# Performance work log

Measured on AMD Instinct MI355X. Metric: run time of the kernel, lower is better.

Reference implementation:

```python
import jax, jax.numpy as jnp
import numpy as np

N_NODES = 50000
N_EDGES = 800000
IN_DIM = 128
HID = 32
HEADS = 4
OUT_DIM = 128
NEG_SLOPE = 0.2


def setup_inputs() -> dict:
    key = jax.random.key(0)
    ks = jax.random.split(key, 10)
    s = lambda fan_in: 1.0 / np.sqrt(fan_in)
    return {
        "x": jax.random.normal(ks[0], (N_NODES, IN_DIM), dtype=jnp.float32),
        "edge_index": jax.random.randint(ks[1], (2, N_EDGES), 0, N_NODES, dtype=jnp.int64),
        # encoder GATConv: in=IN_DIM, out=HID, heads=HEADS (concat)
        "W1": jax.random.normal(ks[2], (IN_DIM, HEADS * HID), dtype=jnp.float32) * s(IN_DIM),
        "att_src1": jax.random.normal(ks[3], (HEADS, HID), dtype=jnp.float32) * s(HID),
        "att_dst1": jax.random.normal(ks[4], (HEADS, HID), dtype=jnp.float32) * s(HID),
        "b1": jnp.zeros((HEADS * HID,), dtype=jnp.float32),
        # decoder GATConv: in=HEADS*HID, out=OUT_DIM, heads=1
        "W2": jax.random.normal(ks[5], (HEADS * HID, OUT_DIM), dtype=jnp.float32) * s(HEADS * HID),
        "att_src2": jax.random.normal(ks[6], (1, OUT_DIM), dtype=jnp.float32) * s(OUT_DIM),
        "att_dst2": jax.random.normal(ks[7], (1, OUT_DIM), dtype=jnp.float32) * s(OUT_DIM),
        "b2": jnp.zeros((OUT_DIM,), dtype=jnp.float32),
    }


def _gat_conv(x, src, dst, W, att_src, att_dst, bias, heads, out_ch):
    """PyG-style GATConv (v1), eval mode (dropout off), self-loops already in src/dst."""
    n = x.shape[0]
    h = (x @ W).reshape(n, heads, out_ch)                 # [N,H,C]
    a_src = jnp.einsum("nhc,hc->nh", h, att_src)          # [N,H]
    a_dst = jnp.einsum("nhc,hc->nh", h, att_dst)          # [N,H]
    e = jax.nn.leaky_relu(a_src[src] + a_dst[dst], NEG_SLOPE)  # [E,H]
    # segment softmax over destination neighborhoods
    e_max = jax.ops.segment_max(e, dst, num_segments=n)   # [N,H]
    e_exp = jnp.exp(e - e_max[dst])
    denom = jax.ops.segment_sum(e_exp, dst, num_segments=n)
    alpha = e_exp / (denom[dst] + 1e-16)                  # [E,H]
    msg = h[src] * alpha[:, :, None]                      # [E,H,C]
    out = jax.ops.segment_sum(msg, dst, num_segments=n)   # [N,H,C]
    return out.reshape(n, heads * out_ch) + bias


def reference(x, edge_index, W1, att_src1, att_dst1, b1, W2, att_src2, att_dst2, b2):
    n = x.shape[0]
    loops = jnp.arange(n, dtype=edge_index.dtype)
    src = jnp.concatenate([edge_index[0], loops])
    dst = jnp.concatenate([edge_index[1], loops])
    z = jax.nn.relu(_gat_conv(x, src, dst, W1, att_src1, att_dst1, b1, HEADS, HID))
    x_hat = jax.nn.relu(_gat_conv(z, src, dst, W2, att_src2, att_dst2, b2, 1, OUT_DIM))
    return x_hat
```

## Files before the change

kernel.cpp:

```cpp
#include <hip/hip_runtime.h>
#include <hip/hip_bf16.h>
#include <cstddef>

#define N_NODES 50000
#define N_EDGES_RAW 800000
#define E_TOT (N_EDGES_RAW + N_NODES)
#define DIM 128
#define NEG_SLOPE 0.2f

#define NBUCK 196
#define CHUNK 4096
#define NBLK_E ((E_TOT + CHUNK - 1) / CHUNK)
#define CONV_BLKS 3125
#define GB 782

typedef __attribute__((ext_vector_type(8))) short bf16x8;
typedef __attribute__((ext_vector_type(4))) float f32x4;

__device__ __forceinline__ ushort f2bf(float f) {
  unsigned u = __float_as_uint(f);
  return (ushort)((u + 0x7FFFu + ((u >> 16) & 1u)) >> 16);
}
__device__ __forceinline__ float bf2f_lo(uint u) {
  return __uint_as_float(u << 16);
}
__device__ __forceinline__ float bf2f_hi(uint u) {
  return __uint_as_float(u & 0xFFFF0000u);
}

__device__ __forceinline__ void get_edge(const int* __restrict__ ei, int is64,
                                         int e, int& s, int& d) {
  if (e >= N_EDGES_RAW) { s = e - N_EDGES_RAW; d = s; return; }
  if (is64) {
    s = ei[2 * (size_t)e];
    d = ei[2 * ((size_t)N_EDGES_RAW + (size_t)e)];
  } else {
    s = ei[e];
    d = ei[N_EDGES_RAW + e];
  }
}

__device__ __forceinline__ int detect_inline(const int* __restrict__ ei,
                                             int* sflag) {
  const int t = threadIdx.x;
  if (t < 64) {
    int hi = ei[2 * t + 1];
    unsigned long long b = __ballot(hi != 0);
    if (t == 0) *sflag = (b == 0ULL) ? 1 : 0;
  }
  __syncthreads();
  return *sflag;
}

__device__ __forceinline__ void prep_one(const float* __restrict__ w,
                                         const float* __restrict__ atts,
                                         const float* __restrict__ attd,
                                         ushort* __restrict__ wtx,
                                         int H, int idx) {
  const int c = idx >> 7, k = idx & 127;
  const int C = 128 / H;
  float v;
  if (c < 128) {
    v = w[k * 128 + c];
  } else if (c < 128 + H) {
    const int hd = c - 128;
    float s = 0.f;
    for (int j = 0; j < C; ++j) s += w[k * 128 + hd * C + j] * atts[hd * C + j];
    v = s;
  } else if (c < 128 + 2 * H) {
    const int hd = c - 128 - H;
    float s = 0.f;
    for (int j = 0; j < C; ++j) s += w[k * 128 + hd * C + j] * attd[hd * C + j];
    v = s;
  } else {
    v = 0.f;
  }
  wtx[idx] = f2bf(v);
}

__global__ __launch_bounds__(256) void mega_setup(
    const float* __restrict__ W1, const float* __restrict__ as1,
    const float* __restrict__ ad1, ushort* __restrict__ wtx1,
    const float* __restrict__ W2, const float* __restrict__ as2,
    const float* __restrict__ ad2, ushort* __restrict__ wtx2,
    const float* __restrict__ x, ushort* __restrict__ x_bf,
    const int* __restrict__ ei, int* __restrict__ hist_mat,
    unsigned* __restrict__ pairs) {
  const int b = blockIdx.x, t = threadIdx.x;
  if (b < 72) {
    prep_one(W1, as1, ad1, wtx1, 4, b * 256 + t);
  } else if (b < 144) {
    prep_one(W2, as2, ad2, wtx2, 1, (b - 72) * 256 + t);
  } else if (b < 144 + CONV_BLKS) {
    const int base = (b - 144) * 2048 + t * 8;
    float4 v0 = *(const float4*)(x + base);
    float4 v1 = *(const float4*)(x + base + 4);
    ushort u[8];
    u[0] = f2bf(v0.x); u[1] = f2bf(v0.y); u[2] = f2bf(v0.z); u[3] = f2bf(v0.w);
    u[4] = f2bf(v1.x); u[5] = f2bf(v1.y); u[6] = f2bf(v1.z); u[7] = f2bf(v1.w);
    *(uint4*)(x_bf + base) = *(const uint4*)u;
  } else {
    __shared__ int hist[NBUCK];
    __shared__ int sflag;
    const int cb = b - 144 - CONV_BLKS;
    if (t < NBUCK) hist[t] = 0;
    const int is64 = detect_inline(ei, &sflag);
    __syncthreads();
    const int e0 = cb * CHUNK;
#pragma unroll
    for (int i = 0; i < CHUNK / 256; ++i) {
      int e = e0 + i * 256 + t;
      if (e < E_TOT) {
        int s, d;
        get_edge(ei, is64, e, s, d);
        pairs[e] = (unsigned)s | ((unsigned)d << 16);
        atomicAdd(&hist[d >> 8], 1);
      }
    }
    __syncthreads();
    if (t < NBUCK) hist_mat[cb * NBUCK + t] = hist[t];
  }
}

__global__ __launch_bounds__(256) void bucket_scatter(
    const unsigned* __restrict__ pairs, const int* __restrict__ hist_mat,
    unsigned* __restrict__ tmp, int* __restrict__ bstart_g) {
  __shared__ int wtot[4];
  __shared__ int sbase[NBUCK];
  __shared__ int shist[NBUCK];
  const int b = blockIdx.x, t = threadIdx.x, lane = t & 63, wid = t >> 6;
  int tot = 0, pre = 0;
  if (t < NBUCK) {
    for (int bb = 0; bb < NBLK_E; ++bb) {
      int v = hist_mat[bb * NBUCK + t];
      pre += (bb < b) ? v : 0;
      tot += v;
    }
    shist[t] = 0;
  }
  int sc = tot;
#pragma unroll
  for (int m = 1; m < 64; m <<= 1) {
    int o = __shfl_up(sc, m, 64);
    if (lane >= m) sc += o;
  }
  if (lane == 63) wtot[wid] = sc;
  __syncthreads();
  int off = 0;
  for (int w = 0; w < wid; ++w) off += wtot[w];
  const int excl = off + sc - tot;
  if (t < NBUCK) sbase[t] = excl + pre;
  if (b == 0) {
    if (t < NBUCK) bstart_g[t] = excl;
    if (t == 255) bstart_g[NBUCK] = off + sc;
  }
  __syncthreads();
  const int e0 = b * CHUNK;
  unsigned pr_[CHUNK / 256];
  int rk[CHUNK / 256];
#pragma unroll
  for (int i = 0; i < CHUNK / 256; ++i) {
    int e = e0 + i * 256 + t;
    if (e < E_TOT) {
      unsigned pr = pairs[e];
      pr_[i] = pr;
      rk[i] = atomicAdd(&shist[pr >> 24], 1);
    }
  }
#pragma unroll
  for (int i = 0; i < CHUNK / 256; ++i) {
    int e = e0 + i * 256 + t;
    if (e < E_TOT) tmp[sbase[pr_[i] >> 24] + rk[i]] = pr_[i];
  }
}

__device__ __forceinline__ void bucket_sort_body(int b,
                                                 const unsigned* __restrict__ tmp,
                                                 const int* __restrict__ bstart,
                                                 int* __restrict__ csr_src,
                                                 int* __restrict__ rp,
                                                 int* __restrict__ deg) {
  __shared__ int cnt[256];
  __shared__ int cur[256];
  __shared__ int wtot2[4];
  const int t = threadIdx.x, lane = t & 63, wid = t >> 6;
  const int p0 = bstart[b], p1 = bstart[b + 1];
  cnt[t] = 0;
  __syncthreads();
  for (int j = p0 + t; j < p1; j += 256) {
    unsigned pr = tmp[j];
    atomicAdd(&cnt[(pr >> 16) & 255u], 1);
  }
  __syncthreads();
  int v = cnt[t];
  int sc = v;
#pragma unroll
  for (int m = 1; m < 64; m <<= 1) {
    int o = __shfl_up(sc, m, 64);
    if (lane >= m) sc += o;
  }
  if (lane == 63) wtot2[wid] = sc;
  __syncthreads();
  int off = 0;
  for (int w = 0; w < wid; ++w) off += wtot2[w];
  const int excl = off + sc - v;
  const int node = b * 256 + t;
  if (node < N_NODES) {
    deg[node] = v;
    rp[node] = p0 + excl;
  }
  cur[t] = excl;
  __syncthreads();
  for (int j = p0 + t; j < p1; j += 256) {
    unsigned pr = tmp[j];
    int ld = (int)((pr >> 16) & 255u);
    int r = atomicAdd(&cur[ld], 1);
    csr_src[p0 + r] = (int)(pr & 0xFFFFu);
  }
}

template <int H>
__device__ __forceinline__ void gemm_att_body(int blk,
                                              const ushort* __restrict__ in_bf,
                                              const ushort* __restrict__ wtx,
                                              ushort* __restrict__ h_bf,
                                              float* __restrict__ a_src,
                                              float* __restrict__ a_dst) {
  const int wid = threadIdx.x >> 6;
  const int lane = threadIdx.x & 63;
  const int tile = blk * 4 + wid;
  if (tile >= N_NODES / 16) return;
  const int row0 = tile * 16;
  const int rA = lane & 15;
  const int g = lane >> 4;

  f32x4 acc[9];
#pragma unroll
  for (int ct = 0; ct < 9; ++ct) acc[ct] = (f32x4){0.f, 0.f, 0.f, 0.f};

#pragma unroll
  for (int ks = 0; ks < 4; ++ks) {
    const int k0 = ks * 32 + g * 8;
    bf16x8 af = *(const bf16x8*)(in_bf + (size_t)(row0 + rA) * DIM + k0);
#pragma unroll
    for (int ct = 0; ct < 9; ++ct) {
      bf16x8 bf = *(const bf16x8*)(wtx + (size_t)(ct * 16 + rA) * 128 + k0);
      acc[ct] = __builtin_amdgcn_mfma_f32_16x16x32_bf16(af, bf, acc[ct], 0, 0, 0);
    }
  }

#pragma unroll
  for (int ct = 0; ct < 8; ++ct) {
#pragma unroll
    for (int r = 0; r < 4; ++r) {
      const int row = row0 + g * 4 + r;
      h_bf[(size_t)row * DIM + ct * 16 + rA] = f2bf(acc[ct][r]);
    }
  }
  if (rA < 2 * H) {
#pragma unroll
    for (int r = 0; r < 4; ++r) {
      const int row = row0 + g * 4 + r;
      if (rA < H)
        a_src[(size_t)row * H + rA] = acc[8][r];
      else
        a_dst[(size_t)row * H + (rA - H)] = acc[8][r];
    }
  }
}

__global__ __launch_bounds__(256) void gemm4_sort(
    const ushort* __restrict__ x_bf, const ushort* __restrict__ wtx1,
    ushort* __restrict__ h_bf, float* __restrict__ a_src,
    float* __restrict__ a_dst, const unsigned* __restrict__ tmp,
    const int* __restrict__ bstart, int* __restrict__ csr_src,
    int* __restrict__ rp, int* __restrict__ deg) {
  if (blockIdx.x < GB)
    gemm_att_body<4>(blockIdx.x, x_bf, wtx1, h_bf, a_src, a_dst);
  else
    bucket_sort_body(blockIdx.x - GB, tmp, bstart, csr_src, rp, deg);
}

__global__ __launch_bounds__(256) void gemm_att1(const ushort* __restrict__ in_bf,
                                                 const ushort* __restrict__ wtx,
                                                 ushort* __restrict__ h_bf,
                                                 float* __restrict__ a_src,
                                                 float* __restrict__ a_dst) {
  gemm_att_body<1>(blockIdx.x, in_bf, wtx, h_bf, a_src, a_dst);
}

template <int H, bool OBF>
__global__ __launch_bounds__(256) void node_agg(const int* __restrict__ rp,
                                                const int* __restrict__ deg,
                                                const int* __restrict__ csr_src,
                                                const ushort* __restrict__ h_bf,
                                                const float* __restrict__ a_src,
                                                const float* __restrict__ a_dst,
                                                const float* __restrict__ bias,
                                                void* __restrict__ outp) {
  const int wid = threadIdx.x >> 6;
  const int lane = threadIdx.x & 63;
  const int node = blockIdx.x * 4 + wid;
  if (node >= N_NODES) return;
  const int ql = lane >> 3;
  const int hl = lane & 7;
  const int head = (H == 4) ? (hl >> 1) : 0;
  const float ad = a_dst[(size_t)node * H + head];
  const int beg = rp[node];
  const int dg = deg[node];
  const int* __restrict__ srcs = csr_src + beg;

  float sden = 0.f;
  float acc[16];
#pragma unroll
  for (int k = 0; k < 16; ++k) acc[k] = 0.f;

  int j = 0;
#pragma unroll 2
  for (; j + 8 <= dg; j += 8) {
    int s = srcs[j + ql];
    float v = a_src[(size_t)s * H + head] + ad;
    v = v > 0.f ? v : NEG_SLOPE * v;
    v = fminf(fmaxf(v, -60.f), 80.f);
    float p = __expf(v);
    const uint4* rowp = (const uint4*)(h_bf + (size_t)s * DIM);
    uint4 h0 = rowp[2 * hl];
    uint4 h1 = rowp[2 * hl + 1];
    sden += p;
    acc[0] += p * bf2f_lo(h0.x);  acc[1] += p * bf2f_hi(h0.x);
    acc[2] += p * bf2f_lo(h0.y);  acc[3] += p * bf2f_hi(h0.y);
    acc[4] += p * bf2f_lo(h0.z);  acc[5] += p * bf2f_hi(h0.z);
    acc[6] += p * bf2f_lo(h0.w);  acc[7] += p * bf2f_hi(h0.w);
    acc[8] += p * bf2f_lo(h1.x);  acc[9] += p * bf2f_hi(h1.x);
    acc[10] += p * bf2f_lo(h1.y); acc[11] += p * bf2f_hi(h1.y);
    acc[12] += p * bf2f_lo(h1.z); acc[13] += p * bf2f_hi(h1.z);
    acc[14] += p * bf2f_lo(h1.w); acc[15] += p * bf2f_hi(h1.w);
  }
  if (j < dg) {
    int jj = j + ql;
    int s = srcs[jj < dg ? jj : (dg - 1)];
    float v = a_src[(size_t)s * H + head] + ad;
    v = v > 0.f ? v : NEG_SLOPE * v;
    v = fminf(fmaxf(v, -60.f), 80.f);
    float p = (jj < dg) ? __expf(v) : 0.f;
    const uint4* rowp = (const uint4*)(h_bf + (size_t)s * DIM);
    uint4 h0 = rowp[2 * hl];
    uint4 h1 = rowp[2 * hl + 1];
    sden += p;
    acc[0] += p * bf2f_lo(h0.x);  acc[1] += p * bf2f_hi(h0.x);
    acc[2] += p * bf2f_lo(h0.y);  acc[3] += p * bf2f_hi(h0.y);
    acc[4] += p * bf2f_lo(h0.z);  acc[5] += p * bf2f_hi(h0.z);
    acc[6] += p * bf2f_lo(h0.w);  acc[7] += p * bf2f_hi(h0.w);
    acc[8] += p * bf2f_lo(h1.x);  acc[9] += p * bf2f_hi(h1.x);
    acc[10] += p * bf2f_lo(h1.y); acc[11] += p * bf2f_hi(h1.y);
    acc[12] += p * bf2f_lo(h1.z); acc[13] += p * bf2f_hi(h1.z);
    acc[14] += p * bf2f_lo(h1.w); acc[15] += p * bf2f_hi(h1.w);
  }

#pragma unroll
  for (int m = 32; m >= 8; m >>= 1) {
    sden += __shfl_xor(sden, m);
#pragma unroll
    for (int k = 0; k < 16; ++k) acc[k] += __shfl_xor(acc[k], m);
  }

  if (lane < 8) {
    const float inv = 1.f / sden;
    float o[16];
#pragma unroll
    for (int q = 0; q < 4; ++q) {
      float4 bv = ((const float4*)bias)[4 * hl + q];
      o[4 * q + 0] = fmaxf(acc[4 * q + 0] * inv + bv.x, 0.f);
      o[4 * q + 1] = fmaxf(acc[4 * q + 1] * inv + bv.y, 0.f);
      o[4 * q + 2] = fmaxf(acc[4 * q + 2] * inv + bv.z, 0.f);
      o[4 * q + 3] = fmaxf(acc[4 * q + 3] * inv + bv.w, 0.f);
    }
    if (OBF) {
      ushort u[16];
#pragma unroll
      for (int k = 0; k < 16; ++k) u[k] = f2bf(o[k]);
      uint4* op = (uint4*)((ushort*)outp + (size_t)node * DIM);
      op[2 * hl] = ((const uint4*)u)[0];
      op[2 * hl + 1] = ((const uint4*)u)[1];
    } else {
      float4* op = (float4*)((float*)outp + (size_t)node * DIM);
#pragma unroll
      for (int q = 0; q < 4; ++q)
        op[4 * hl + q] = make_float4(o[4 * q], o[4 * q + 1], o[4 * q + 2], o[4 * q + 3]);
    }
  }
}

extern "C" void kernel_launch(void* const* d_in, const int* in_sizes, int n_in,
                              void* d_out, int out_size, void* d_ws, size_t ws_size,
                              hipStream_t stream) {
  const float* x   = (const float*)d_in[0];
  const int*   ei  = (const int*)d_in[1];
  const float* W1  = (const float*)d_in[2];
  const float* as1 = (const float*)d_in[3];
  const float* ad1 = (const float*)d_in[4];
  const float* b1  = (const float*)d_in[5];
  const float* W2  = (const float*)d_in[6];
  const float* as2 = (const float*)d_in[7];
  const float* ad2 = (const float*)d_in[8];
  const float* b2  = (const float*)d_in[9];
  float* out = (float*)d_out;

  char* ws = (char*)d_ws;
  const size_t F_H = (size_t)N_NODES * DIM;
  ushort*   h_bf    = (ushort*)ws;
  ushort*   z_bf    = h_bf + F_H;
  ushort*   x_bf    = z_bf + F_H;
  float*    a_src   = (float*)(x_bf + F_H);
  float*    a_dst   = a_src + 200000;
  int*      deg     = (int*)(a_dst + 200000);
  int*      rp      = deg + N_NODES;
  int*      csr_src = rp + N_NODES;
  unsigned* tmp     = (unsigned*)(csr_src + E_TOT);
  unsigned* pairs   = tmp + E_TOT;
  int*      hist_mat= (int*)(pairs + E_TOT);
  int*      bstart  = hist_mat + NBLK_E * NBUCK;
  ushort*   wtx1    = (ushort*)(bstart + NBUCK + 3);
  ushort*   wtx2    = wtx1 + 144 * 128;

  const int MEGA = 144 + CONV_BLKS + NBLK_E;

  hipLaunchKernelGGL(mega_setup, dim3(MEGA), dim3(256), 0, stream,
                     W1, as1, ad1, wtx1, W2, as2, ad2, wtx2, x, x_bf, ei,
                     hist_mat, pairs);
  hipLaunchKernelGGL(bucket_scatter, dim3(NBLK_E), dim3(256), 0, stream,
                     pairs, hist_mat, tmp, bstart);
  hipLaunchKernelGGL(gemm4_sort, dim3(GB + NBUCK), dim3(256), 0, stream,
                     x_bf, wtx1, h_bf, a_src, a_dst, tmp, bstart, csr_src, rp, deg);
  hipLaunchKernelGGL((node_agg<4, true>), dim3((N_NODES + 3) / 4), dim3(256), 0,
                     stream, rp, deg, csr_src, h_bf, a_src, a_dst, b1, z_bf);

  hipLaunchKernelGGL(gemm_att1, dim3(GB), dim3(256), 0, stream,
                     z_bf, wtx2, h_bf, a_src, a_dst);
  hipLaunchKernelGGL((node_agg<1, false>), dim3((N_NODES + 3) / 4), dim3(256), 0,
                     stream, rp, deg, csr_src, h_bf, a_src, a_dst, b2, out);
}
```

Before: 164.5 us.

## Remap node aggregation to per-edge full-wave row loads with LDS-staged attention

The node aggregation kernel previously gave each wave 8 edges at once, with 8 lanes per edge row, and then reduced 16 accumulators across lanes with shuffles. It now computes the attention weights for up to 64 edges once (one lane per edge, all heads from a single float4 load) and stages them with the source indices in LDS. All 64 lanes then walk the edges together, each reading a 4-byte slice of the source row. This removes the large shuffle reduction and the repeated per-head a_src loads. In exchange each lane issues narrower loads, the edges are processed serially, and extra LDS traffic is added.

```diff
diff --git a/kernel.cpp b/kernel.cpp
--- a/kernel.cpp
+++ b/kernel.cpp
@@ -298,96 +298,87 @@
                                                 const float* __restrict__ a_dst,
                                                 const float* __restrict__ bias,
                                                 void* __restrict__ outp) {
+  __shared__ float p_lds[4][H][64];
+  __shared__ int s_lds[4][64];
   const int wid = threadIdx.x >> 6;
   const int lane = threadIdx.x & 63;
   const int node = blockIdx.x * 4 + wid;
   if (node >= N_NODES) return;
-  const int ql = lane >> 3;
-  const int hl = lane & 7;
-  const int head = (H == 4) ? (hl >> 1) : 0;
-  const float ad = a_dst[(size_t)node * H + head];
+  const int head = (H == 4) ? (lane >> 4) : 0;
   const int beg = rp[node];
   const int dg = deg[node];
   const int* __restrict__ srcs = csr_src + beg;
 
-  float sden = 0.f;
-  float acc[16];
-#pragma unroll
-  for (int k = 0; k < 16; ++k) acc[k] = 0.f;
-
-  int j = 0;
-#pragma unroll 2
-  for (; j + 8 <= dg; j += 8) {
-    int s = srcs[j + ql];
-    float v = a_src[(size_t)s * H + head] + ad;
-    v = v > 0.f ? v : NEG_SLOPE * v;
-    v = fminf(fmaxf(v, -60.f), 80.f);
-    float p = __expf(v);
-    const uint4* rowp = (const uint4*)(h_bf + (size_t)s * DIM);
-    uint4 h0 = rowp[2 * hl];
-    uint4 h1 = rowp[2 * hl + 1];
-    sden += p;
-    acc[0] += p * bf2f_lo(h0.x);  acc[1] += p * bf2f_hi(h0.x);
-    acc[2] += p * bf2f_lo(h0.y);  acc[3] += p * bf2f_hi(h0.y);
-    acc[4] += p * bf2f_lo(h0.z);  acc[5] += p * bf2f_hi(h0.z);
-    acc[6] += p * bf2f_lo(h0.w);  acc[7] += p * bf2f_hi(h0.w);
-    acc[8] += p * bf2f_lo(h1.x);  acc[9] += p * bf2f_hi(h1.x);
-    acc[10] += p * bf2f_lo(h1.y); acc[11] += p * bf2f_hi(h1.y);
-    acc[12] += p * bf2f_lo(h1.z); acc[13] += p * bf2f_hi(h1.z);
-    acc[14] += p * bf2f_lo(h1.w); acc[15] += p * bf2f_hi(h1.w);
-  }
-  if (j < dg) {
-    int jj = j + ql;
-    int s = srcs[jj < dg ? jj : (dg - 1)];
-    float v = a_src[(size_t)s * H + head] + ad;
-    v = v > 0.f ? v : NEG_SLOPE * v;
-    v = fminf(fmaxf(v, -60.f), 80.f);
-    float p = (jj < dg) ? __expf(v) : 0.f;
-    const uint4* rowp = (const uint4*)(h_bf + (size_t)s * DIM);
-    uint4 h0 = rowp[2 * hl];
-    uint4 h1 = rowp[2 * hl + 1];
-    sden += p;
-    acc[0] += p * bf2f_lo(h0.x);  acc[1] += p * bf2f_hi(h0.x);
-    acc[2] += p * bf2f_lo(h0.y);  acc[3] += p * bf2f_hi(h0.y);
-    acc[4] += p * bf2f_lo(h0.z);  acc[5] += p * bf2f_hi(h0.z);
-    acc[6] += p * bf2f_lo(h0.w);  acc[7] += p * bf2f_hi(h0.w);
-    acc[8] += p * bf2f_lo(h1.x);  acc[9] += p * bf2f_hi(h1.x);
-    acc[10] += p * bf2f_lo(h1.y); acc[11] += p * bf2f_hi(h1.y);
-    acc[12] += p * bf2f_lo(h1.z); acc[13] += p * bf2f_hi(h1.z);
-    acc[14] += p * bf2f_lo(h1.w); acc[15] += p * bf2f_hi(h1.w);
-  }
-
-#pragma unroll
-  for (int m = 32; m >= 8; m >>= 1) {
-    sden += __shfl_xor(sden, m);
-#pragma unroll
-    for (int k = 0; k < 16; ++k) acc[k] += __shfl_xor(acc[k], m);
-  }
-
-  if (lane < 8) {
-    const float inv = 1.f / sden;
-    float o[16];
-#pragma unroll
-    for (int q = 0; q < 4; ++q) {
-      float4 bv = ((const float4*)bias)[4 * hl + q];
-      o[4 * q + 0] = fmaxf(acc[4 * q + 0] * inv + bv.x, 0.f);
-      o[4 * q + 1] = fmaxf(acc[4 * q + 1] * inv + bv.y, 0.f);
-      o[4 * q + 2] = fmaxf(acc[4 * q + 2] * inv + bv.z, 0.f);
-      o[4 * q + 3] = fmaxf(acc[4 * q + 3] * inv + bv.w, 0.f);
-    }
-    if (OBF) {
-      ushort u[16];
-#pragma unroll
-      for (int k = 0; k < 16; ++k) u[k] = f2bf(o[k]);
-      uint4* op = (uint4*)((ushort*)outp + (size_t)node * DIM);
-      op[2 * hl] = ((const uint4*)u)[0];
-      op[2 * hl + 1] = ((const uint4*)u)[1];
-    } else {
-      float4* op = (float4*)((float*)outp + (size_t)node * DIM);
-#pragma unroll
-      for (int q = 0; q < 4; ++q)
-        op[4 * hl + q] = make_float4(o[4 * q], o[4 * q + 1], o[4 * q + 2], o[4 * q + 3]);
-    }
+  float ad[H];
+#pragma unroll
+  for (int h = 0; h < H; ++h) ad[h] = a_dst[(size_t)node * H + h];
+
+  float sden[H];
+#pragma unroll
+  for (int h = 0; h < H; ++h) sden[h] = 0.f;
+  float ax = 0.f, ay = 0.f;
+
+  for (int c0 = 0; c0 < dg; c0 += 64) {
+    const int cnt = min(64, dg - c0);
+    if (lane < cnt) {
+      int s = srcs[c0 + lane];
+      s_lds[wid][lane] = s;
+      if (H == 4) {
+        float4 as4 = ((const float4*)a_src)[s];
+        float vv[4] = {as4.x, as4.y, as4.z, as4.w};
+#pragma unroll
+        for (int h = 0; h < 4; ++h) {
+          float v = vv[h] + ad[h];
+          v = v > 0.f ? v : NEG_SLOPE * v;
+          v = fminf(fmaxf(v, -60.f), 80.f);
+          float p = __expf(v);
+          sden[h] += p;
+          p_lds[wid][h][lane] = p;
+        }
+      } else {
+        float v = a_src[s] + ad[0];
+        v = v > 0.f ? v : NEG_SLOPE * v;
+        v = fminf(fmaxf(v, -60.f), 80.f);
+        float p = __expf(v);
+        sden[0] += p;
+        p_lds[wid][0][lane] = p;
+      }
+    }
+    int j = 0;
+    for (; j + 8 <= cnt; j += 8) {
+#pragma unroll
+      for (int u = 0; u < 8; ++u) {
+        int s = s_lds[wid][j + u];
+        float p = p_lds[wid][head][j + u];
+        uint hv = *(const uint*)(h_bf + (size_t)s * DIM + 2 * lane);
+        ax += p * bf2f_lo(hv);
+        ay += p * bf2f_hi(hv);
+      }
+    }
+    for (; j < cnt; ++j) {
+      int s = s_lds[wid][j];
+      float p = p_lds[wid][head][j];
+      uint hv = *(const uint*)(h_bf + (size_t)s * DIM + 2 * lane);
+      ax += p * bf2f_lo(hv);
+      ay += p * bf2f_hi(hv);
+    }
+  }
+
+#pragma unroll
+  for (int h = 0; h < H; ++h) {
+#pragma unroll
+    for (int m = 1; m < 64; m <<= 1) sden[h] += __shfl_xor(sden[h], m);
+  }
+  const float inv = 1.f / sden[head];
+
+  float2 bv = ((const float2*)bias)[lane];
+  float ox = fmaxf(ax * inv + bv.x, 0.f);
+  float oy = fmaxf(ay * inv + bv.y, 0.f);
+  if (OBF) {
+    uint u = (uint)f2bf(ox) | ((uint)f2bf(oy) << 16);
+    ((uint*)((ushort*)outp + (size_t)node * DIM))[lane] = u;
+  } else {
+    ((float2*)((float*)outp + (size_t)node * DIM))[lane] = make_float2(ox, oy);
   }
 }
 
```

Result: no change. 165.6 us (+0.7%).
